# Kernel tuning notes

Measured on AMD Instinct MI355X. Metric: run time of the kernel, lower is better.

The kernel has to match this reference:

```python
import jax, jax.numpy as jnp
import numpy as np

L = 128          # lifted_dim
NS = 50000       # source nodes
NT = 50000       # target nodes
E = 640000       # edges
SLOPE = 0.01     # cfg.leaky_slope (torch LeakyReLU default)
EPS = 1e-5       # BatchNorm eps


def _glorot(key, shape):
    fan_in, fan_out = shape[0], shape[1]
    lim = np.sqrt(6.0 / (fan_in + fan_out)).astype(np.float32)
    return jax.random.uniform(key, shape, jnp.float32, -lim, lim)


def setup_inputs() -> dict:
    key = jax.random.key(0)
    ks = jax.random.split(key, 16)
    x_s = jax.random.normal(ks[0], (NS, L), jnp.float32)
    x_t = jax.random.normal(ks[1], (NT, L), jnp.float32)
    edge_index = jax.random.randint(ks[2], (2, E), 0, NT, jnp.int64)
    edge_attr = jax.random.normal(ks[3], (E, L), jnp.float32)
    x_u = jax.random.normal(ks[4], (L,), jnp.float32)
    M = 2 * L  # message_dim
    U = 4 * L  # update_dim
    params = {
        'W1': _glorot(ks[5], (M, M)), 'b1': jnp.zeros((M,), jnp.float32),
        'W2': _glorot(ks[6], (M, M)), 'b2': jnp.zeros((M,), jnp.float32),
        'U1': _glorot(ks[7], (U, U)), 'c1': jnp.zeros((U,), jnp.float32),
        'U2': _glorot(ks[8], (U, L)), 'c2': jnp.zeros((L,), jnp.float32),
        'gamma': jnp.ones((L,), jnp.float32), 'beta': jnp.zeros((L,), jnp.float32),
    }
    return dict(x_s=x_s, x_t=x_t, edge_index=edge_index, edge_attr=edge_attr, x_u=x_u, **params)


def reference(x_s, x_t, edge_index, edge_attr, x_u,
              W1, b1, W2, b2, U1, c1, U2, c2, gamma, beta):
    src, tgt = edge_index[0], edge_index[1]
    # edge messages: gather source features + edge attrs -> 2-layer MLP
    msg = jnp.concatenate([x_s[src], edge_attr], axis=1)          # [E, 2L]
    msg = jax.nn.leaky_relu(msg @ W1 + b1, negative_slope=SLOPE)
    msg = msg @ W2 + b2                                           # [E, 2L]
    # scatter-add aggregation onto target nodes
    agg = jax.ops.segment_sum(msg, tgt, num_segments=x_t.shape[0])  # [NT, 2L]
    # node update
    xu = jnp.broadcast_to(x_u[None, :], (x_t.shape[0], x_u.shape[0]))
    h = jnp.concatenate([x_t, agg, xu], axis=-1)                  # [NT, 4L]
    h = jax.nn.leaky_relu(h @ U1 + c1, negative_slope=SLOPE)
    h = h @ U2 + c2                                               # [NT, L]
    # BatchNorm1d (training mode: batch statistics, biased variance)
    mu = jnp.mean(h, axis=0)
    var = jnp.var(h, axis=0)
    return gamma * (h - mu) * jax.lax.rsqrt(var + EPS) + beta
```

## Files before the change

### kernel.cpp

```cpp
#include <hip/hip_runtime.h>

typedef unsigned int u32;
typedef unsigned short u16;
typedef __attribute__((ext_vector_type(8))) short short8;
typedef __attribute__((ext_vector_type(8))) unsigned short ushort8v;
typedef __attribute__((ext_vector_type(4))) unsigned short ushort4v;
typedef __attribute__((ext_vector_type(4))) float f32x4;

#define NSRC 50000
#define NTGT 50000
#define NEDGE 640000
#define LDIM 128
#define SLOPE 0.01f

#define MFMA(a, b, c) __builtin_amdgcn_mfma_f32_16x16x32_bf16((a), (b), (c), 0, 0, 0)

__device__ __forceinline__ u16 f2bf(float f) {
  union { float f; u32 u; } v; v.f = f;
  u32 r = v.u + 0x7FFFu + ((v.u >> 16) & 1u);
  return (u16)(r >> 16);
}
__device__ __forceinline__ float bf2f(u16 h) {
  union { u32 u; float f; } v; v.u = ((u32)h) << 16; return v.f;
}

__global__ void k_w2b(const float* __restrict__ W2, const float* __restrict__ U1,
                      float* __restrict__ w2b) {
  const int i = blockIdx.x;
  const int j = threadIdx.x;
  const float* __restrict__ u = U1 + (size_t)128 * 512;
  float a0 = 0.f, a1 = 0.f;
#pragma unroll 8
  for (int k = 0; k < 256; ++k) {
    float w = W2[(size_t)i * 256 + k];
    a0 += w * u[(size_t)k * 512 + j];
    a1 += w * u[(size_t)k * 512 + j + 256];
  }
  w2b[(size_t)i * 512 + j] = a0;
  w2b[(size_t)i * 512 + j + 256] = a1;
}

__global__ void k_bias(const float* __restrict__ U1, const float* __restrict__ xu,
                       const float* __restrict__ b2, const float* __restrict__ c1,
                       float* __restrict__ c1e, float* __restrict__ vb) {
  const int j = threadIdx.x;
  float s = c1[j];
#pragma unroll 4
  for (int k = 0; k < 128; ++k) s += xu[k] * U1[(size_t)(384 + k) * 512 + j];
  float v = 0.f;
#pragma unroll 4
  for (int k = 0; k < 256; ++k) v += b2[k] * U1[(size_t)(128 + k) * 512 + j];
  c1e[j] = s;
  vb[j] = v;
}

__global__ void k_prep(const float* __restrict__ W1, const float* __restrict__ U1,
                       const float* __restrict__ U2, const float* __restrict__ w2b,
                       u16* __restrict__ w1a, u16* __restrict__ w1b,
                       u16* __restrict__ u1e, u16* __restrict__ u2p) {
  int id = blockIdx.x * 256 + threadIdx.x;
  int lane = id & 63, quad = (lane >> 4), l16 = lane & 15;
  if (id < 4096) {
    int g = id >> 6;
    int kc = g >> 4, cb = g & 15;
    const float* s = W1 + (size_t)(kc * 32 + quad * 8) * 256 + cb * 16 + l16;
    ushort8v p;
#pragma unroll
    for (int j = 0; j < 8; ++j) p[j] = f2bf(s[(size_t)j * 256]);
    *(ushort8v*)(w1a + ((size_t)g * 64 + lane) * 8) = p;
  } else if (id < 8192) {
    int g = (id - 4096) >> 6;
    int kc = g >> 4, cb = g & 15;
    const float* s = W1 + (size_t)(128 + kc * 32 + quad * 8) * 256 + cb * 16 + l16;
    ushort8v p;
#pragma unroll
    for (int j = 0; j < 8; ++j) p[j] = f2bf(s[(size_t)j * 256]);
    *(ushort8v*)(w1b + ((size_t)g * 64 + lane) * 8) = p;
  } else if (id < 32768) {
    int g = (id - 8192) >> 6;
    int kc = g >> 5, cb = g & 31;
    int col = cb * 16 + l16;
    ushort8v p;
#pragma unroll
    for (int j = 0; j < 8; ++j) {
      int row = kc * 32 + quad * 8 + j;
      float v = (row < 128) ? U1[(size_t)row * 512 + col]
                            : w2b[(size_t)(row - 128) * 512 + col];
      p[j] = f2bf(v);
    }
    *(ushort8v*)(u1e + ((size_t)g * 64 + lane) * 8) = p;
  } else if (id < 40960) {
    int g = (id - 32768) >> 6;
    int kc = g >> 3, cb = g & 7;
    const float* s = U2 + (size_t)(kc * 32 + quad * 8) * 128 + cb * 16 + l16;
    ushort8v p;
#pragma unroll
    for (int j = 0; j < 8; ++j) p[j] = f2bf(s[(size_t)j * 128]);
    *(ushort8v*)(u2p + ((size_t)g * 64 + lane) * 8) = p;
  }
}

__global__ void k_count(const int* __restrict__ tgt, int* __restrict__ cnt,
                        int* __restrict__ rank) {
  int e = blockIdx.x * 256 + threadIdx.x;
  if (e < NEDGE) rank[e] = atomicAdd(&cnt[tgt[e]], 1);
}

__global__ void k_scan(const int* __restrict__ cnt, int* __restrict__ rowstart) {
  __shared__ int part[1024];
  int tid = threadIdx.x;
  int base = tid * 49;
  int s = 0;
  for (int i = 0; i < 49; ++i) { int idx = base + i; if (idx < NTGT) s += cnt[idx]; }
  part[tid] = s;
  __syncthreads();
  for (int off = 1; off < 1024; off <<= 1) {
    int v = (tid >= off) ? part[tid - off] : 0;
    __syncthreads();
    part[tid] += v;
    __syncthreads();
  }
  int run = (tid > 0) ? part[tid - 1] : 0;
  for (int i = 0; i < 49; ++i) {
    int idx = base + i;
    if (idx < NTGT) { rowstart[idx] = run; run += cnt[idx]; }
  }
  if (tid == 1023) rowstart[NTGT] = part[1023];
}

__global__ void k_pos(const int* __restrict__ tgt, const int* __restrict__ rowstart,
                      int* __restrict__ pos) {
  int e = blockIdx.x * 256 + threadIdx.x;
  if (e < NEDGE) pos[e] = rowstart[tgt[e]] + pos[e];
}

__global__ __launch_bounds__(256, 3) void k_pgemm(
    const float* __restrict__ xs, const u16* __restrict__ w1ap,
    const float* __restrict__ b1, u16* __restrict__ P) {
  __shared__ u16 At[64][136];
  __shared__ u16 Ot[64][264];
  const int tid = threadIdx.x;
  const int base = blockIdx.x * 64;
  {
    const int et = tid >> 2, p = tid & 3;
    const int row = base + et;
    u16* dst = &At[et][p * 32];
    if (row < NSRC) {
      const float4* f4 = (const float4*)(xs + (size_t)row * LDIM + p * 32);
#pragma unroll
      for (int i = 0; i < 4; ++i) {
        float4 a = f4[2 * i], b = f4[2 * i + 1];
        ushort8v pk = { f2bf(a.x), f2bf(a.y), f2bf(a.z), f2bf(a.w),
                        f2bf(b.x), f2bf(b.y), f2bf(b.z), f2bf(b.w) };
        *(ushort8v*)(dst + i * 8) = pk;
      }
    } else {
      ushort8v z = {0, 0, 0, 0, 0, 0, 0, 0};
#pragma unroll
      for (int i = 0; i < 4; ++i) *(ushort8v*)(dst + i * 8) = z;
    }
  }
  __syncthreads();

  const int lane = tid & 63, wid = tid >> 6;
  const int quad = lane >> 4, l16 = lane & 15;
  const int colb = wid * 64;
  const short8* __restrict__ wf = (const short8*)w1ap;

  f32x4 acc[4][4];
#pragma unroll
  for (int a = 0; a < 4; ++a)
#pragma unroll
    for (int b = 0; b < 4; ++b) acc[a][b] = (f32x4){0.f, 0.f, 0.f, 0.f};
#pragma unroll
  for (int kc = 0; kc < 4; ++kc) {
    short8 af[4], bfr[4];
#pragma unroll
    for (int ct = 0; ct < 4; ++ct)
      bfr[ct] = wf[(size_t)(kc * 16 + wid * 4 + ct) * 64 + lane];
#pragma unroll
    for (int rt = 0; rt < 4; ++rt)
      af[rt] = *(const short8*)&At[rt * 16 + l16][kc * 32 + quad * 8];
#pragma unroll
    for (int rt = 0; rt < 4; ++rt)
#pragma unroll
      for (int ct = 0; ct < 4; ++ct)
        acc[rt][ct] = MFMA(af[rt], bfr[ct], acc[rt][ct]);
  }
#pragma unroll
  for (int ct = 0; ct < 4; ++ct) {
    int col = colb + ct * 16 + l16;
    float bias = b1[col];
#pragma unroll
    for (int rt = 0; rt < 4; ++rt)
#pragma unroll
      for (int r = 0; r < 4; ++r) {
        int row = rt * 16 + quad * 4 + r;
        Ot[row][col] = f2bf(acc[rt][ct][r] + bias);
      }
  }
  __syncthreads();
  {
    const int et = tid >> 2, p = tid & 3;
    const int row = base + et;
    if (row < NSRC) {
      u16* dst = P + (size_t)row * 256 + p * 64;
      const u16* sl = &Ot[et][p * 64];
#pragma unroll
      for (int i = 0; i < 8; ++i)
        *(ushort8v*)(dst + i * 8) = *(const ushort8v*)(sl + i * 8);
    }
  }
}

__global__ __launch_bounds__(256, 3) void k_edge(
    const float* __restrict__ ea, const int* __restrict__ srcp,
    const u16* __restrict__ Pg, const u16* __restrict__ w1bp,
    const int* __restrict__ pos, u16* __restrict__ tbuf) {
  __shared__ u16 At[64][136];
  __shared__ u16 Pt[64][264];
  const int tid = threadIdx.x;
  const int ebase = blockIdx.x * 64;

  {
    const int et = tid >> 2, p = tid & 3;
    if (p < 2) {
      const float4* f4 = (const float4*)(ea + (size_t)(ebase + et) * LDIM + p * 64);
      u16* dst = &At[et][p * 64];
#pragma unroll
      for (int i = 0; i < 8; ++i) {
        float4 a = f4[2 * i], b = f4[2 * i + 1];
        ushort8v pk = { f2bf(a.x), f2bf(a.y), f2bf(a.z), f2bf(a.w),
                        f2bf(b.x), f2bf(b.y), f2bf(b.z), f2bf(b.w) };
        *(ushort8v*)(dst + i * 8) = pk;
      }
    } else {
      int sidx = srcp[ebase + et];
      const ushort8v* pr = (const ushort8v*)(Pg + (size_t)sidx * 256 + (p - 2) * 128);
      u16* dst = &Pt[et][(p - 2) * 128];
#pragma unroll
      for (int i = 0; i < 16; ++i) *(ushort8v*)(dst + i * 8) = pr[i];
    }
  }
  __syncthreads();

  const int lane = tid & 63, wid = tid >> 6;
  const int quad = lane >> 4, l16 = lane & 15;
  const int colb = wid * 64;
  const short8* __restrict__ wf = (const short8*)w1bp;

  f32x4 acc[4][4];
#pragma unroll
  for (int a = 0; a < 4; ++a)
#pragma unroll
    for (int b = 0; b < 4; ++b) acc[a][b] = (f32x4){0.f, 0.f, 0.f, 0.f};
#pragma unroll
  for (int kc = 0; kc < 4; ++kc) {
    short8 af[4], bfr[4];
#pragma unroll
    for (int ct = 0; ct < 4; ++ct)
      bfr[ct] = wf[(size_t)(kc * 16 + wid * 4 + ct) * 64 + lane];
#pragma unroll
    for (int rt = 0; rt < 4; ++rt)
      af[rt] = *(const short8*)&At[rt * 16 + l16][kc * 32 + quad * 8];
#pragma unroll
    for (int rt = 0; rt < 4; ++rt)
#pragma unroll
      for (int ct = 0; ct < 4; ++ct)
        acc[rt][ct] = MFMA(af[rt], bfr[ct], acc[rt][ct]);
  }
#pragma unroll
  for (int ct = 0; ct < 4; ++ct) {
    int col = colb + ct * 16 + l16;
#pragma unroll
    for (int rt = 0; rt < 4; ++rt)
#pragma unroll
      for (int r = 0; r < 4; ++r) {
        int row = rt * 16 + quad * 4 + r;
        float v = acc[rt][ct][r] + bf2f(Pt[row][col]);
        v = v > 0.f ? v : SLOPE * v;
        Pt[row][col] = f2bf(v);
      }
  }
  __syncthreads();

  {
    const int et = tid >> 2, p = tid & 3;
    const int gp = pos[ebase + et];
    u16* dst = tbuf + (size_t)gp * 256 + p * 64;
    const u16* sl = &Pt[et][p * 64];
#pragma unroll
    for (int i = 0; i < 8; ++i)
      *(ushort8v*)(dst + i * 8) = *(const ushort8v*)(sl + i * 8);
  }
}

__global__ __launch_bounds__(256, 4) void k_node(
    const float* __restrict__ xt, const u16* __restrict__ tbuf,
    const int* __restrict__ rowstart, const u16* __restrict__ u1e,
    const u16* __restrict__ u2p, const float* __restrict__ c1e,
    const float* __restrict__ vb, const float* __restrict__ c2,
    float* __restrict__ h2, float* __restrict__ stats) {
  __shared__ u16 ain[32][520];
  __shared__ float sdeg[32];
  const int tid = threadIdx.x;
  const int lane = tid & 63, wid = tid >> 6;
  const int quad = lane >> 4, l16 = lane & 15;
  const int tbase = blockIdx.x * 32;

  for (int s = wid; s < 32; s += 4) {
    int t = tbase + s;
    if (t < NTGT) {
      if (lane < 32) {
        float4 v = ((const float4*)(xt + (size_t)t * LDIM))[lane];
        ushort4v p = { f2bf(v.x), f2bf(v.y), f2bf(v.z), f2bf(v.w) };
        *(ushort4v*)&ain[s][lane * 4] = p;
      }
      int rs = rowstart[t], re = rowstart[t + 1];
      if (lane == 0) sdeg[s] = (float)(re - rs);
      float acc8[8] = {0.f, 0.f, 0.f, 0.f, 0.f, 0.f, 0.f, 0.f};
      const u16* mb = tbuf + ((size_t)rs + (lane >> 5)) * 256 + (lane & 31) * 8;
      int n = re - rs, nfull = n & ~1;
      for (int r = 0; r < nfull; r += 2) {
        ushort8v m = *(const ushort8v*)(mb + (size_t)r * 256);
#pragma unroll
        for (int j = 0; j < 8; ++j) acc8[j] += bf2f(m[j]);
      }
      if (n & 1) {
        if (lane < 32) {
          ushort8v m = *(const ushort8v*)(tbuf + (size_t)(re - 1) * 256 + lane * 8);
#pragma unroll
          for (int j = 0; j < 8; ++j) acc8[j] += bf2f(m[j]);
        }
      }
#pragma unroll
      for (int j = 0; j < 8; ++j) acc8[j] += __shfl_down(acc8[j], 32);
      if (lane < 32) {
        ushort8v p;
#pragma unroll
        for (int j = 0; j < 8; ++j) p[j] = f2bf(acc8[j]);
        *(ushort8v*)&ain[s][128 + lane * 8] = p;
      }
    } else {
      ushort8v z = {0, 0, 0, 0, 0, 0, 0, 0};
      *(ushort8v*)&ain[s][lane * 8] = z;
      if (lane == 0) sdeg[s] = 0.f;
    }
  }
  __syncthreads();

  const short8* __restrict__ u1f = (const short8*)u1e;
  const short8* __restrict__ u2f = (const short8*)u2p;

  f32x4 acc[2][2][4];
#pragma unroll
  for (int h = 0; h < 2; ++h)
#pragma unroll
    for (int a = 0; a < 2; ++a)
#pragma unroll
      for (int b = 0; b < 4; ++b) acc[h][a][b] = (f32x4){0.f, 0.f, 0.f, 0.f};

#pragma unroll 2
  for (int kc = 0; kc < 12; ++kc) {
    short8 af[2];
#pragma unroll
    for (int rt = 0; rt < 2; ++rt)
      af[rt] = *(const short8*)&ain[rt * 16 + l16][kc * 32 + quad * 8];
#pragma unroll
    for (int h = 0; h < 2; ++h) {
      short8 bfr[4];
#pragma unroll
      for (int ct = 0; ct < 4; ++ct)
        bfr[ct] = u1f[(size_t)(kc * 32 + h * 16 + wid * 4 + ct) * 64 + lane];
#pragma unroll
      for (int rt = 0; rt < 2; ++rt)
#pragma unroll
        for (int ct = 0; ct < 4; ++ct)
          acc[h][rt][ct] = MFMA(af[rt], bfr[ct], acc[h][rt][ct]);
    }
  }
  __syncthreads();
#pragma unroll
  for (int h = 0; h < 2; ++h)
#pragma unroll
    for (int ct = 0; ct < 4; ++ct) {
      int col = h * 256 + wid * 64 + ct * 16 + l16;
      float cb = c1e[col], vbb = vb[col];
#pragma unroll
      for (int rt = 0; rt < 2; ++rt)
#pragma unroll
        for (int r = 0; r < 4; ++r) {
          int row = rt * 16 + quad * 4 + r;
          float v = acc[h][rt][ct][r] + cb + sdeg[row] * vbb;
          v = v > 0.f ? v : SLOPE * v;
          ain[row][col] = f2bf(v);
        }
    }
  __syncthreads();

  const int colb2 = wid * 32;
  f32x4 acc2[2][2];
#pragma unroll
  for (int a = 0; a < 2; ++a)
#pragma unroll
    for (int b = 0; b < 2; ++b) acc2[a][b] = (f32x4){0.f, 0.f, 0.f, 0.f};
#pragma unroll 4
  for (int kc = 0; kc < 16; ++kc) {
    short8 af[2], bfr[2];
#pragma unroll
    for (int ct = 0; ct < 2; ++ct)
      bfr[ct] = u2f[(size_t)(kc * 8 + wid * 2 + ct) * 64 + lane];
#pragma unroll
    for (int rt = 0; rt < 2; ++rt)
      af[rt] = *(const short8*)&ain[rt * 16 + l16][kc * 32 + quad * 8];
#pragma unroll
    for (int rt = 0; rt < 2; ++rt)
#pragma unroll
      for (int ct = 0; ct < 2; ++ct)
        acc2[rt][ct] = MFMA(af[rt], bfr[ct], acc2[rt][ct]);
  }
  float s1[2] = {0.f, 0.f}, s2[2] = {0.f, 0.f};
#pragma unroll
  for (int ct = 0; ct < 2; ++ct) {
    int col = colb2 + ct * 16 + l16;
    float cb = c2[col];
#pragma unroll
    for (int rt = 0; rt < 2; ++rt)
#pragma unroll
      for (int r = 0; r < 4; ++r) {
        int row = rt * 16 + quad * 4 + r;
        int t = tbase + row;
        if (t < NTGT) {
          float v = acc2[rt][ct][r] + cb;
          h2[(size_t)t * LDIM + col] = v;
          s1[ct] += v; s2[ct] += v * v;
        }
      }
  }
#pragma unroll
  for (int ct = 0; ct < 2; ++ct) {
    float a = s1[ct], b = s2[ct];
    a += __shfl_down(a, 32); b += __shfl_down(b, 32);
    a += __shfl_down(a, 16); b += __shfl_down(b, 16);
    if (lane < 16) {
      atomicAdd(&stats[colb2 + ct * 16 + l16], a);
      atomicAdd(&stats[128 + colb2 + ct * 16 + l16], b);
    }
  }
}

__global__ void k_bnfin(const float* __restrict__ stats, const float* __restrict__ gamma,
                        const float* __restrict__ beta, float* __restrict__ ss) {
  int c = threadIdx.x;
  if (c < 128) {
    float mu = stats[c] * (1.0f / NTGT);
    float var = stats[128 + c] * (1.0f / NTGT) - mu * mu;
    float rs = rsqrtf(var + 1e-5f);
    float sc = gamma[c] * rs;
    ss[c] = sc;
    ss[128 + c] = beta[c] - mu * sc;
  }
}

__global__ void k_bnapply(const float* __restrict__ h2, const float* __restrict__ ss,
                          float* __restrict__ out) {
  int i = blockIdx.x * 256 + threadIdx.x;
  const int total = NTGT * LDIM / 4;
  const float4* h4 = (const float4*)h2;
  const float4* sc4 = (const float4*)ss;
  const float4* sh4 = (const float4*)(ss + 128);
  float4* o4 = (float4*)out;
  for (; i < total; i += gridDim.x * 256) {
    int cg = i & 31;
    float4 h = h4[i], sc = sc4[cg], sh = sh4[cg];
    float4 r = { h.x * sc.x + sh.x, h.y * sc.y + sh.y,
                 h.z * sc.z + sh.z, h.w * sc.w + sh.w };
    o4[i] = r;
  }
}

extern "C" void kernel_launch(void* const* d_in, const int* in_sizes, int n_in,
                              void* d_out, int out_size, void* d_ws, size_t ws_size,
                              hipStream_t stream) {
  (void)in_sizes; (void)n_in; (void)out_size; (void)ws_size;
  const float* xs    = (const float*)d_in[0];
  const float* xt    = (const float*)d_in[1];
  const int*   ei    = (const int*)d_in[2];
  const float* ea    = (const float*)d_in[3];
  const float* xu    = (const float*)d_in[4];
  const float* W1    = (const float*)d_in[5];
  const float* b1    = (const float*)d_in[6];
  const float* W2    = (const float*)d_in[7];
  const float* b2    = (const float*)d_in[8];
  const float* U1    = (const float*)d_in[9];
  const float* c1    = (const float*)d_in[10];
  const float* U2    = (const float*)d_in[11];
  const float* c2    = (const float*)d_in[12];
  const float* gamma = (const float*)d_in[13];
  const float* beta  = (const float*)d_in[14];

  char* ws = (char*)d_ws;
  u16* w1a   = (u16*)(ws + 0x000000);
  u16* w1b   = (u16*)(ws + 0x010000);
  u16* u1e   = (u16*)(ws + 0x020000);
  u16* u2p   = (u16*)(ws + 0x080000);
  float* w2b = (float*)(ws + 0x0A0000);
  float* c1e = (float*)(ws + 0x120000);
  float* vbv = (float*)(ws + 0x120800);
  int* cnt   = (int*)(ws + 0x130000);
  int* rowst = (int*)(ws + 0x161000);
  int* pos   = (int*)(ws + 0x192000);
  float* stats = (float*)(ws + 0x410000);
  float* ss    = stats + 256;
  u16*   Pbuf = (u16*)(ws + 0x412000);
  float* h2   = (float*)(ws + 0x412000);
  u16*   tbuf = (u16*)(ws + 0x1C80000);

  const int* srcp = ei;
  const int* tgtp = ei + NEDGE;

  hipMemsetAsync(cnt, 0, NTGT * 4, stream);
  hipMemsetAsync(stats, 0, 256 * 4, stream);
  k_w2b<<<256, 256, 0, stream>>>(W2, U1, w2b);
  k_bias<<<1, 512, 0, stream>>>(U1, xu, b2, c1, c1e, vbv);
  k_prep<<<160, 256, 0, stream>>>(W1, U1, U2, w2b, w1a, w1b, u1e, u2p);
  k_count<<<2500, 256, 0, stream>>>(tgtp, cnt, pos);
  k_scan<<<1, 1024, 0, stream>>>(cnt, rowst);
  k_pos<<<2500, 256, 0, stream>>>(tgtp, rowst, pos);
  k_pgemm<<<782, 256, 0, stream>>>(xs, w1a, b1, Pbuf);
  k_edge<<<10000, 256, 0, stream>>>(ea, srcp, Pbuf, w1b, pos, tbuf);
  k_node<<<1563, 256, 0, stream>>>(xt, tbuf, rowst, u1e, u2p, c1e, vbv, c2, h2, stats);
  k_bnfin<<<1, 128, 0, stream>>>(stats, gamma, beta, ss);
  k_bnapply<<<6250, 256, 0, stream>>>(h2, ss, (float*)d_out);
}
```

Baseline: 974.1 us.

## Process edges in target-sorted order and reduce segments in-block into fp32 agg

Builds an inverse permutation so the edge kernel processes edges sorted by target. Each block reduces runs of equal targets in shared memory and writes the segment sums straight into an fp32 aggregate buffer, using atomics only for segments that touch the first or last row of the block. This replaces the per-edge bf16 message buffer that the node kernel gathered and summed, cutting a large write plus re-read. The cost is gathering edge_attr rows in permuted order, a serial 64-step column loop, an extra memset of the aggregate buffer, and atomics at block boundaries.

Result: faster. 905.1 us (-7.1%).

```diff
diff --git a/kernel.cpp b/kernel.cpp
--- a/kernel.cpp
+++ b/kernel.cpp
@@ -132,6 +132,11 @@
                       int* __restrict__ pos) {
   int e = blockIdx.x * 256 + threadIdx.x;
   if (e < NEDGE) pos[e] = rowstart[tgt[e]] + pos[e];
+}
+
+__global__ void k_inv(const int* __restrict__ pos, int* __restrict__ order) {
+  int e = blockIdx.x * 256 + threadIdx.x;
+  if (e < NEDGE) order[pos[e]] = e;
 }
 
 __global__ __launch_bounds__(256, 3) void k_pgemm(
@@ -215,17 +220,21 @@
 
 __global__ __launch_bounds__(256, 3) void k_edge(
     const float* __restrict__ ea, const int* __restrict__ srcp,
+    const int* __restrict__ tgtp, const int* __restrict__ order,
     const u16* __restrict__ Pg, const u16* __restrict__ w1bp,
-    const int* __restrict__ pos, u16* __restrict__ tbuf) {
+    float* __restrict__ agg) {
   __shared__ u16 At[64][136];
   __shared__ u16 Pt[64][264];
+  __shared__ int s_tgt[64];
   const int tid = threadIdx.x;
-  const int ebase = blockIdx.x * 64;
+  const int base = blockIdx.x * 64;
 
   {
     const int et = tid >> 2, p = tid & 3;
+    const int e = order[base + et];
+    if (p == 0) s_tgt[et] = tgtp[e];
     if (p < 2) {
-      const float4* f4 = (const float4*)(ea + (size_t)(ebase + et) * LDIM + p * 64);
+      const float4* f4 = (const float4*)(ea + (size_t)e * LDIM + p * 64);
       u16* dst = &At[et][p * 64];
 #pragma unroll
       for (int i = 0; i < 8; ++i) {
@@ -235,7 +244,7 @@
         *(ushort8v*)(dst + i * 8) = pk;
       }
     } else {
-      int sidx = srcp[ebase + et];
+      int sidx = srcp[e];
       const ushort8v* pr = (const ushort8v*)(Pg + (size_t)sidx * 256 + (p - 2) * 128);
       u16* dst = &Pt[et][(p - 2) * 128];
 #pragma unroll
@@ -285,18 +294,26 @@
   __syncthreads();
 
   {
-    const int et = tid >> 2, p = tid & 3;
-    const int gp = pos[ebase + et];
-    u16* dst = tbuf + (size_t)gp * 256 + p * 64;
-    const u16* sl = &Pt[et][p * 64];
-#pragma unroll
-    for (int i = 0; i < 8; ++i)
-      *(ushort8v*)(dst + i * 8) = *(const ushort8v*)(sl + i * 8);
+    const int col = tid;
+    float accv = 0.f;
+    int prev = s_tgt[0];
+    int segstart = 0;
+    for (int r = 0; r < 64; ++r) {
+      int t = s_tgt[r];
+      if (t != prev) {
+        float* dst = agg + (size_t)prev * 256 + col;
+        if (segstart == 0) atomicAdd(dst, accv);
+        else *dst = accv;
+        accv = 0.f; prev = t; segstart = r;
+      }
+      accv += bf2f(Pt[r][col]);
+    }
+    atomicAdd(agg + (size_t)prev * 256 + col, accv);
   }
 }
 
 __global__ __launch_bounds__(256, 4) void k_node(
-    const float* __restrict__ xt, const u16* __restrict__ tbuf,
+    const float* __restrict__ xt, const float* __restrict__ agg,
     const int* __restrict__ rowstart, const u16* __restrict__ u1e,
     const u16* __restrict__ u2p, const float* __restrict__ c1e,
     const float* __restrict__ vb, const float* __restrict__ c2,
@@ -316,31 +333,10 @@
         ushort4v p = { f2bf(v.x), f2bf(v.y), f2bf(v.z), f2bf(v.w) };
         *(ushort4v*)&ain[s][lane * 4] = p;
       }
-      int rs = rowstart[t], re = rowstart[t + 1];
-      if (lane == 0) sdeg[s] = (float)(re - rs);
-      float acc8[8] = {0.f, 0.f, 0.f, 0.f, 0.f, 0.f, 0.f, 0.f};
-      const u16* mb = tbuf + ((size_t)rs + (lane >> 5)) * 256 + (lane & 31) * 8;
-      int n = re - rs, nfull = n & ~1;
-      for (int r = 0; r < nfull; r += 2) {
-        ushort8v m = *(const ushort8v*)(mb + (size_t)r * 256);
-#pragma unroll
-        for (int j = 0; j < 8; ++j) acc8[j] += bf2f(m[j]);
-      }
-      if (n & 1) {
-        if (lane < 32) {
-          ushort8v m = *(const ushort8v*)(tbuf + (size_t)(re - 1) * 256 + lane * 8);
-#pragma unroll
-          for (int j = 0; j < 8; ++j) acc8[j] += bf2f(m[j]);
-        }
-      }
-#pragma unroll
-      for (int j = 0; j < 8; ++j) acc8[j] += __shfl_down(acc8[j], 32);
-      if (lane < 32) {
-        ushort8v p;
-#pragma unroll
-        for (int j = 0; j < 8; ++j) p[j] = f2bf(acc8[j]);
-        *(ushort8v*)&ain[s][128 + lane * 8] = p;
-      }
+      if (lane == 0) sdeg[s] = (float)(rowstart[t + 1] - rowstart[t]);
+      float4 v = ((const float4*)(agg + (size_t)t * 256))[lane];
+      ushort4v p = { f2bf(v.x), f2bf(v.y), f2bf(v.z), f2bf(v.w) };
+      *(ushort4v*)&ain[s][128 + lane * 4] = p;
     } else {
       ushort8v z = {0, 0, 0, 0, 0, 0, 0, 0};
       *(ushort8v*)&ain[s][lane * 8] = z;
@@ -510,26 +506,29 @@
   int* cnt   = (int*)(ws + 0x130000);
   int* rowst = (int*)(ws + 0x161000);
   int* pos   = (int*)(ws + 0x192000);
-  float* stats = (float*)(ws + 0x410000);
+  float* stats = (float*)(ws + 0x404000);
   float* ss    = stats + 256;
-  u16*   Pbuf = (u16*)(ws + 0x412000);
-  float* h2   = (float*)(ws + 0x412000);
-  u16*   tbuf = (u16*)(ws + 0x1C80000);
+  int* order = (int*)(ws + 0x405000);
+  float* agg = (float*)(ws + 0x680000);
+  u16*   Pbuf = (u16*)(ws + 0x3760000);
+  float* h2   = (float*)(ws + 0x3760000);
 
   const int* srcp = ei;
   const int* tgtp = ei + NEDGE;
 
   hipMemsetAsync(cnt, 0, NTGT * 4, stream);
   hipMemsetAsync(stats, 0, 256 * 4, stream);
+  hipMemsetAsync(agg, 0, (size_t)NTGT * 256 * 4, stream);
   k_w2b<<<256, 256, 0, stream>>>(W2, U1, w2b);
   k_bias<<<1, 512, 0, stream>>>(U1, xu, b2, c1, c1e, vbv);
   k_prep<<<160, 256, 0, stream>>>(W1, U1, U2, w2b, w1a, w1b, u1e, u2p);
   k_count<<<2500, 256, 0, stream>>>(tgtp, cnt, pos);
   k_scan<<<1, 1024, 0, stream>>>(cnt, rowst);
   k_pos<<<2500, 256, 0, stream>>>(tgtp, rowst, pos);
+  k_inv<<<2500, 256, 0, stream>>>(pos, order);
   k_pgemm<<<782, 256, 0, stream>>>(xs, w1a, b1, Pbuf);
-  k_edge<<<10000, 256, 0, stream>>>(ea, srcp, Pbuf, w1b, pos, tbuf);
-  k_node<<<1563, 256, 0, stream>>>(xt, tbuf, rowst, u1e, u2p, c1e, vbv, c2, h2, stats);
+  k_edge<<<10000, 256, 0, stream>>>(ea, srcp, tgtp, order, Pbuf, w1b, agg);
+  k_node<<<1563, 256, 0, stream>>>(xt, agg, rowst, u1e, u2p, c1e, vbv, c2, h2, stats);
   k_bnfin<<<1, 128, 0, stream>>>(stats, gamma, beta, ss);
   k_bnapply<<<6250, 256, 0, stream>>>(h2, ss, (float*)d_out);
 }
```
